# Optimization experiments

Measured on AMD Instinct MI355X. Metric: run time of the kernel, lower is better.

## Reference

```python
import jax, jax.numpy as jnp
import numpy as np

N_HEADS, D_MODEL, DK, DV = 16, 1024, 64, 64
B, S = 4, 2048


def setup_inputs() -> dict:
    key = jax.random.key(0)
    ks = jax.random.split(key, 7)
    scale = 1.0 / np.sqrt(D_MODEL)
    return {
        "Q": jax.random.normal(ks[0], (B, S, D_MODEL), dtype=jnp.float32),
        "K": jax.random.normal(ks[1], (B, S, D_MODEL), dtype=jnp.float32),
        "V": jax.random.normal(ks[2], (B, S, D_MODEL), dtype=jnp.float32),
        # Linear weights stored as [in, out] so y = x @ W (equivalent to torch x @ W.T)
        "w_q": jax.random.normal(ks[3], (D_MODEL, N_HEADS * DK), dtype=jnp.float32) * scale,
        "w_k": jax.random.normal(ks[4], (D_MODEL, N_HEADS * DK), dtype=jnp.float32) * scale,
        "w_v": jax.random.normal(ks[5], (D_MODEL, N_HEADS * DV), dtype=jnp.float32) * scale,
        "w_o": jax.random.normal(ks[6], (N_HEADS * DV, D_MODEL), dtype=jnp.float32) * scale,
    }


def reference(Q, K, V, w_q, w_k, w_v, w_o):
    b, s, _ = Q.shape
    # projections -> [B, H, S, d]
    q = (Q @ w_q).reshape(b, s, N_HEADS, DK).transpose(0, 2, 1, 3)
    k = (K @ w_k).reshape(b, s, N_HEADS, DK).transpose(0, 2, 1, 3)
    v = (V @ w_v).reshape(b, s, N_HEADS, DV).transpose(0, 2, 1, 3)
    # scaled dot-product attention, full [B,H,S,S] scores (matches source)
    scores = jnp.einsum("bhqd,bhkd->bhqk", q, k) / jnp.sqrt(jnp.float32(DK))
    attn = jax.nn.softmax(scores, axis=-1)
    x = jnp.einsum("bhqk,bhkd->bhqd", attn, v)
    x = x.transpose(0, 2, 1, 3).reshape(b, s, N_HEADS * DV)
    return x @ w_o
```

## Files before the change

kernel.cpp:

```cpp
#include <hip/hip_runtime.h>
#include <stdint.h>

#define B_   4
#define S_   2048
#define H_   16
#define D_   64
#define DM_  1024
#define NTOK (B_ * S_)

typedef __attribute__((ext_vector_type(8))) short short8;
typedef __attribute__((ext_vector_type(4))) float floatx4;

__device__ inline unsigned short f2bf(float f) {
  unsigned int u = __float_as_uint(f);
  u += 0x7FFFu + ((u >> 16) & 1u);
  return (unsigned short)(u >> 16);
}

__device__ inline floatx4 mfma_bf16(short8 a, short8 b, floatx4 c) {
  return __builtin_amdgcn_mfma_f32_16x16x32_bf16(a, b, c, 0, 0, 0);
}

__device__ inline unsigned int pack_bf2(float lo, float hi) {
  return __builtin_amdgcn_perm(__float_as_uint(hi), __float_as_uint(lo), 0x07060302u);
}

__device__ inline void gload_lds16(const unsigned short* g, unsigned short* l) {
  __builtin_amdgcn_global_load_lds(
      (const __attribute__((address_space(1))) unsigned int*)g,
      (__attribute__((address_space(3))) unsigned int*)l, 16, 0, 0);
}

__global__ __launch_bounds__(256) void cast3_kernel(const float* __restrict__ Q,
                                                    const float* __restrict__ Kf,
                                                    const float* __restrict__ V,
                                                    unsigned short* __restrict__ qB,
                                                    unsigned short* __restrict__ kB,
                                                    unsigned short* __restrict__ vB) {
  const float* in = blockIdx.z == 0 ? Q : blockIdx.z == 1 ? Kf : V;
  unsigned short* out = blockIdx.z == 0 ? qB : blockIdx.z == 1 ? kB : vB;
  const int n4 = NTOK * DM_ / 4;
  for (int i = blockIdx.x * 256 + threadIdx.x; i < n4; i += gridDim.x * 256) {
    float4 v = ((const float4*)in)[i];
    ushort4 o;
    o.x = f2bf(v.x); o.y = f2bf(v.y); o.z = f2bf(v.z); o.w = f2bf(v.w);
    ((ushort4*)out)[i] = o;
  }
}

__global__ __launch_bounds__(256) void wt_kernel(const float* __restrict__ w0,
                                                 const float* __restrict__ w1,
                                                 const float* __restrict__ w2,
                                                 const float* __restrict__ w3,
                                                 unsigned short* __restrict__ o0,
                                                 unsigned short* __restrict__ o1,
                                                 unsigned short* __restrict__ o2,
                                                 unsigned short* __restrict__ o3) {
  __shared__ unsigned short T[64 * 68];
  const float* w = blockIdx.z == 0 ? w0 : blockIdx.z == 1 ? w1 : blockIdx.z == 2 ? w2 : w3;
  unsigned short* o = blockIdx.z == 0 ? o0 : blockIdx.z == 1 ? o1 : blockIdx.z == 2 ? o2 : o3;
  const int tid = threadIdx.x;
  const int R0 = blockIdx.y * 64;
  const int C0 = blockIdx.x * 64;
  for (int it = 0; it < 16; it++) {
    int lr = it * 4 + (tid >> 6), lc = tid & 63;
    T[lc * 68 + lr] = f2bf(w[(size_t)(R0 + lr) * 1024 + C0 + lc]);
  }
  __syncthreads();
  for (int it = 0; it < 2; it++) {
    int orow = it * 32 + (tid >> 3), oc = (tid & 7) * 8;
    union { ushort4 h[2]; short8 v8; } u;
    u.h[0] = *(const ushort4*)(T + orow * 68 + oc);
    u.h[1] = *(const ushort4*)(T + orow * 68 + oc + 4);
    *(short8*)(o + (size_t)(C0 + orow) * 1024 + R0 + oc) = u.v8;
  }
}

__global__ __launch_bounds__(512) void gemm256_kernel(
    const unsigned short* __restrict__ A0, const unsigned short* __restrict__ A1,
    const unsigned short* __restrict__ A2,
    const unsigned short* __restrict__ Bt0, const unsigned short* __restrict__ Bt1,
    const unsigned short* __restrict__ Bt2,
    void* __restrict__ C0, void* __restrict__ C1, void* __restrict__ C2,
    int mode_z0, float scale_z0) {
  constexpr int K = 1024;
  __shared__ __align__(16) unsigned short As[2][256 * 64];
  __shared__ __align__(16) unsigned short Bs[2][128 * 64];

  const int tid  = threadIdx.x;
  const int wave = tid >> 6, lane = tid & 63;
  const int quad = lane >> 4, l16 = lane & 15;
  const int wm = wave >> 2, wn = wave & 3;

  const int g  = blockIdx.x * gridDim.y + blockIdx.y;
  const int z  = g >> 8;
  const int rz = g & 255;
  const int mb = rz >> 3, nb = rz & 7;
  const int m0 = mb * 256, n0 = nb * 128;

  const unsigned short* A  = z == 0 ? A0  : z == 1 ? A1  : A2;
  const unsigned short* BT = z == 0 ? Bt0 : z == 1 ? Bt1 : Bt2;
  void* Cout               = z == 0 ? C0  : z == 1 ? C1  : C2;
  const int   mode  = z == 0 ? mode_z0 : (z == 2 ? 2 : 0);
  const float scale = z == 0 ? scale_z0 : 1.0f;

  floatx4 acc[8][2] = {};

#define STAGE256(k0, buf)                                              \
  do {                                                                 \
    _Pragma("unroll")                                                  \
    for (int p = 0; p < 4; p++) {                                      \
      int si = p * 512 + tid;                                          \
      int rr = si >> 3;                                                \
      int gc = (si & 7) ^ (rr & 7);                                    \
      gload_lds16(A + (size_t)(m0 + rr) * K + (k0) + gc * 8,           \
                  As[buf] + (size_t)(p * 512 + wave * 64) * 8);        \
    }                                                                  \
    _Pragma("unroll")                                                  \
    for (int p = 0; p < 2; p++) {                                      \
      int si = p * 512 + tid;                                          \
      int rr = si >> 3;                                                \
      int gc = (si & 7) ^ (rr & 7);                                    \
      gload_lds16(BT + (size_t)(n0 + rr) * K + (k0) + gc * 8,          \
                  Bs[buf] + (size_t)(p * 512 + wave * 64) * 8);        \
    }                                                                  \
  } while (0)

  STAGE256(0, 0);

  int cur = 0;
  for (int k0 = 0; k0 < K; k0 += 64) {
    __syncthreads();

    if (k0 + 64 < K) STAGE256(k0 + 64, cur ^ 1);

    short8 bfr[2][2];
#pragma unroll
    for (int n = 0; n < 2; n++)
#pragma unroll
      for (int kk = 0; kk < 2; kk++) {
        int rb = wn * 32 + n * 16 + l16;
        int j = kk * 4 + quad;
        bfr[n][kk] = *(const short8*)(Bs[cur] + rb * 64 + (j ^ (rb & 7)) * 8);
      }
#pragma unroll
    for (int f = 0; f < 8; f++) {
      int ra = wm * 128 + f * 16 + l16;
      short8 a0 = *(const short8*)(As[cur] + ra * 64 + ((quad)     ^ (ra & 7)) * 8);
      short8 a1 = *(const short8*)(As[cur] + ra * 64 + ((4 + quad) ^ (ra & 7)) * 8);
#pragma unroll
      for (int n = 0; n < 2; n++) {
        acc[f][n] = mfma_bf16(a0, bfr[n][0], acc[f][n]);
        acc[f][n] = mfma_bf16(a1, bfr[n][1], acc[f][n]);
      }
    }
    cur ^= 1;
  }
#undef STAGE256

#pragma unroll
  for (int f = 0; f < 8; f++)
#pragma unroll
    for (int n = 0; n < 2; n++)
#pragma unroll
      for (int r = 0; r < 4; r++) {
        int gm = m0 + wm * 128 + f * 16 + quad * 4 + r;
        int gn = n0 + wn * 32 + n * 16 + l16;
        float val = acc[f][n][r] * scale;
        if (mode == 0) {
          int b = gm >> 11, s = gm & 2047;
          int h = gn >> 6,  d = gn & 63;
          ((unsigned short*)Cout)[((size_t)((b * H_ + h) * S_ + s) << 6) + d] = f2bf(val);
        } else if (mode == 1) {
          ((float*)Cout)[((size_t)gm << 10) + gn] = val;
        } else {
          int b = gm >> 11, s = gm & 2047;
          int h = gn >> 6,  d = gn & 63;
          int p = ((s & 63) >> 4) + (s & 15) * 4;
          ((unsigned short*)Cout)[(((size_t)(b * H_ + h) * 64 + d) << 11) + (s & ~63) + p] = f2bf(val);
        }
      }
}

__global__ __launch_bounds__(512, 4) void attn_kernel(const unsigned short* __restrict__ q,
                                                      const unsigned short* __restrict__ k,
                                                      const unsigned short* __restrict__ vT,
                                                      unsigned short* __restrict__ X) {
  __shared__ unsigned short Ks[2][64 * 64];
  __shared__ unsigned short Vt[2][64 * 64];
  __shared__ unsigned short Ps[8][16 * 72];

  const int tid  = threadIdx.x;
  const int wave = tid >> 6, lane = tid & 63;
  const int quad = lane >> 4, l16 = lane & 15;
  const int bh = blockIdx.x * 8 + (blockIdx.y >> 3);
  const int q0 = (blockIdx.y & 7) * 256;

  const unsigned short* qh = q  + (size_t)bh * S_ * 64;
  const unsigned short* kh = k  + (size_t)bh * S_ * 64;
  const unsigned short* vh = vT + (size_t)bh * 64 * S_;

  const int sr  = tid >> 3;
  const int sgc = (tid & 7) ^ (sr & 7);

  short8 qf[2][2];
  for (int qt = 0; qt < 2; qt++) {
    int row = q0 + wave * 32 + qt * 16 + l16;
    for (int kk = 0; kk < 2; kk++)
      qf[qt][kk] = *(const short8*)(qh + (size_t)row * 64 + kk * 32 + quad * 8);
  }

  short8 onesb = {};
  if (l16 == 0)
    for (int e = 0; e < 8; e++) onesb[e] = (short)0x3F80;

  const floatx4 fz = {};
  floatx4 O[2][4] = {};
  floatx4 lacc[2] = {};

  gload_lds16(kh + (size_t)sr * 64 + sgc * 8,       Ks[0] + (size_t)(wave * 64) * 8);
  gload_lds16(vh + (size_t)sr * S_ + 0 + sgc * 8,   Vt[0] + (size_t)(wave * 64) * 8);

  int cur = 0;
  for (int j0 = 0; j0 < S_; j0 += 64) {
    __syncthreads();

    if (j0 + 64 < S_) {
      int nxt = cur ^ 1;
      gload_lds16(kh + (size_t)(j0 + 64 + sr) * 64 + sgc * 8,
                  Ks[nxt] + (size_t)(wave * 64) * 8);
      gload_lds16(vh + (size_t)sr * S_ + (j0 + 64) + sgc * 8,
                  Vt[nxt] + (size_t)(wave * 64) * 8);
    }

    short8 kf[4][2];
    for (int jf = 0; jf < 4; jf++)
      for (int kk = 0; kk < 2; kk++) {
        int sl = (kk * 4 + quad) ^ (l16 & 7);
        kf[jf][kk] = *(const short8*)(Ks[cur] + (jf * 16 + l16) * 64 + sl * 8);
      }

    unsigned short* pw = Ps[wave];
    short8 pa[2][2];
    for (int qt = 0; qt < 2; qt++) {
      floatx4 s[4];
      for (int jf = 0; jf < 4; jf++) {
        s[jf] = mfma_bf16(qf[qt][0], kf[jf][0], fz);
        s[jf] = mfma_bf16(qf[qt][1], kf[jf][1], s[jf]);
      }
      for (int r = 0; r < 4; r++) {
        float e0 = __builtin_amdgcn_exp2f(s[0][r]);
        float e1 = __builtin_amdgcn_exp2f(s[1][r]);
        float e2 = __builtin_amdgcn_exp2f(s[2][r]);
        float e3 = __builtin_amdgcn_exp2f(s[3][r]);
        uint2 pk;
        pk.x = pack_bf2(e0, e1);
        pk.y = pack_bf2(e2, e3);
        *(uint2*)(pw + (quad * 4 + r) * 72 + l16 * 4) = pk;
      }
      pa[qt][0] = *(const short8*)(pw + l16 * 72 + quad * 8);
      pa[qt][1] = *(const short8*)(pw + l16 * 72 + 32 + quad * 8);
      lacc[qt] = mfma_bf16(pa[qt][0], onesb, lacc[qt]);
      lacc[qt] = mfma_bf16(pa[qt][1], onesb, lacc[qt]);
    }

    for (int df = 0; df < 4; df++) {
      int sl0 = quad ^ (l16 & 7);
      int sl1 = (4 + quad) ^ (l16 & 7);
      short8 v0 = *(const short8*)(Vt[cur] + (df * 16 + l16) * 64 + sl0 * 8);
      short8 v1 = *(const short8*)(Vt[cur] + (df * 16 + l16) * 64 + sl1 * 8);
      for (int qt = 0; qt < 2; qt++) {
        O[qt][df] = mfma_bf16(pa[qt][0], v0, O[qt][df]);
        O[qt][df] = mfma_bf16(pa[qt][1], v1, O[qt][df]);
      }
    }
    cur ^= 1;
  }

  const int b = bh >> 4, h = bh & 15;
  for (int qt = 0; qt < 2; qt++)
    for (int r = 0; r < 4; r++) {
      float lsum = __shfl(lacc[qt][r], (lane & 48));
      float inv = 1.0f / lsum;
      int row = q0 + wave * 32 + qt * 16 + quad * 4 + r;
      unsigned short* dst = X + ((size_t)(b * S_ + row) << 10) + h * 64;
      for (int df = 0; df < 4; df++)
        dst[df * 16 + l16] = f2bf(O[qt][df][r] * inv);
    }
}

extern "C" void kernel_launch(void* const* d_in, const int* in_sizes, int n_in,
                              void* d_out, int out_size, void* d_ws, size_t ws_size,
                              hipStream_t stream) {
  const float* Q  = (const float*)d_in[0];
  const float* K  = (const float*)d_in[1];
  const float* V  = (const float*)d_in[2];
  const float* wq = (const float*)d_in[3];
  const float* wk = (const float*)d_in[4];
  const float* wv = (const float*)d_in[5];
  const float* wo = (const float*)d_in[6];

  char* ws = (char*)d_ws;
  unsigned short* buf0 = (unsigned short*)ws;
  unsigned short* wqT  = (unsigned short*)(ws + (size_t)(16 << 20));
  unsigned short* wkT  = (unsigned short*)(ws + (size_t)(18 << 20));
  unsigned short* wvT  = (unsigned short*)(ws + (size_t)(20 << 20));
  unsigned short* woT  = (unsigned short*)(ws + (size_t)(22 << 20));
  unsigned short* qP   = (unsigned short*)(ws + (size_t)(24 << 20));
  unsigned short* kP   = (unsigned short*)(ws + (size_t)(40 << 20));
  unsigned short* vTg  = (unsigned short*)(ws + (size_t)(56 << 20));

  unsigned short* qB = (unsigned short*)d_out;
  unsigned short* kB = qB + (size_t)8 * 1024 * 1024;
  unsigned short* vB = buf0;

  const float SC = 0.18033688011112043f;

  wt_kernel<<<dim3(16, 16, 4), dim3(256), 0, stream>>>(wq, wk, wv, wo, wqT, wkT, wvT, woT);

  cast3_kernel<<<dim3(2048, 1, 3), dim3(256), 0, stream>>>(Q, K, V, qB, kB, vB);

  gemm256_kernel<<<dim3(8, 96), dim3(512), 0, stream>>>(
      qB, kB, vB, wqT, wkT, wvT, qP, kP, vTg, 0, SC);

  attn_kernel<<<dim3(8, 64), dim3(512), 0, stream>>>(qP, kP, vTg, buf0);

  gemm256_kernel<<<dim3(8, 32), dim3(512), 0, stream>>>(
      buf0, buf0, buf0, woT, woT, woT, d_out, d_out, d_out, 1, 1.0f);
}
```

Measured before the change: 357.7 us.

## Triple-buffer GEMM K-loop with explicit vmcnt waits and merge prep kernels

The projection GEMM moves from double to triple buffering in LDS, keeping two K-tiles of global->LDS loads in flight. It replaces __syncthreads with counted s_waitcnt vmcnt plus raw barriers. The weight-transpose and input-cast kernels are fused into one launch to cut launch overhead. LDS use grows to 144KB per block, and the hand-counted waits must match the number of issued loads.

```diff
diff --git a/kernel.cpp b/kernel.cpp
--- a/kernel.cpp
+++ b/kernel.cpp
@@ -31,37 +31,39 @@
       (__attribute__((address_space(3))) unsigned int*)l, 16, 0, 0);
 }
 
-__global__ __launch_bounds__(256) void cast3_kernel(const float* __restrict__ Q,
-                                                    const float* __restrict__ Kf,
-                                                    const float* __restrict__ V,
-                                                    unsigned short* __restrict__ qB,
-                                                    unsigned short* __restrict__ kB,
-                                                    unsigned short* __restrict__ vB) {
-  const float* in = blockIdx.z == 0 ? Q : blockIdx.z == 1 ? Kf : V;
-  unsigned short* out = blockIdx.z == 0 ? qB : blockIdx.z == 1 ? kB : vB;
-  const int n4 = NTOK * DM_ / 4;
-  for (int i = blockIdx.x * 256 + threadIdx.x; i < n4; i += gridDim.x * 256) {
-    float4 v = ((const float4*)in)[i];
-    ushort4 o;
-    o.x = f2bf(v.x); o.y = f2bf(v.y); o.z = f2bf(v.z); o.w = f2bf(v.w);
-    ((ushort4*)out)[i] = o;
-  }
-}
-
-__global__ __launch_bounds__(256) void wt_kernel(const float* __restrict__ w0,
-                                                 const float* __restrict__ w1,
-                                                 const float* __restrict__ w2,
-                                                 const float* __restrict__ w3,
-                                                 unsigned short* __restrict__ o0,
-                                                 unsigned short* __restrict__ o1,
-                                                 unsigned short* __restrict__ o2,
-                                                 unsigned short* __restrict__ o3) {
+__global__ __launch_bounds__(256) void prep_kernel(
+    const float* __restrict__ Q, const float* __restrict__ Kf,
+    const float* __restrict__ V,
+    const float* __restrict__ w0, const float* __restrict__ w1,
+    const float* __restrict__ w2, const float* __restrict__ w3,
+    unsigned short* __restrict__ qB, unsigned short* __restrict__ kB,
+    unsigned short* __restrict__ vB,
+    unsigned short* __restrict__ o0, unsigned short* __restrict__ o1,
+    unsigned short* __restrict__ o2, unsigned short* __restrict__ o3) {
   __shared__ unsigned short T[64 * 68];
-  const float* w = blockIdx.z == 0 ? w0 : blockIdx.z == 1 ? w1 : blockIdx.z == 2 ? w2 : w3;
-  unsigned short* o = blockIdx.z == 0 ? o0 : blockIdx.z == 1 ? o1 : blockIdx.z == 2 ? o2 : o3;
+  const int z = blockIdx.z;
   const int tid = threadIdx.x;
-  const int R0 = blockIdx.y * 64;
-  const int C0 = blockIdx.x * 64;
+
+  if (z < 3) {
+    const float* in = z == 0 ? Q : z == 1 ? Kf : V;
+    unsigned short* out = z == 0 ? qB : z == 1 ? kB : vB;
+    const int n4 = NTOK * DM_ / 4;
+    for (int i = blockIdx.x * 256 + tid; i < n4; i += gridDim.x * 256) {
+      float4 v = ((const float4*)in)[i];
+      ushort4 o;
+      o.x = f2bf(v.x); o.y = f2bf(v.y); o.z = f2bf(v.z); o.w = f2bf(v.w);
+      ((ushort4*)out)[i] = o;
+    }
+    return;
+  }
+
+  const int bx = blockIdx.x;
+  if (bx >= 1024) return;
+  const int wsel = bx >> 8, tile = bx & 255;
+  const float* w = wsel == 0 ? w0 : wsel == 1 ? w1 : wsel == 2 ? w2 : w3;
+  unsigned short* o = wsel == 0 ? o0 : wsel == 1 ? o1 : wsel == 2 ? o2 : o3;
+  const int R0 = (tile >> 4) * 64;
+  const int C0 = (tile & 15) * 64;
   for (int it = 0; it < 16; it++) {
     int lr = it * 4 + (tid >> 6), lc = tid & 63;
     T[lc * 68 + lr] = f2bf(w[(size_t)(R0 + lr) * 1024 + C0 + lc]);
@@ -84,8 +86,9 @@
     void* __restrict__ C0, void* __restrict__ C1, void* __restrict__ C2,
     int mode_z0, float scale_z0) {
   constexpr int K = 1024;
-  __shared__ __align__(16) unsigned short As[2][256 * 64];
-  __shared__ __align__(16) unsigned short Bs[2][128 * 64];
+  constexpr int NKT = K / 64;
+  __shared__ __align__(16) unsigned short As[3][256 * 64];
+  __shared__ __align__(16) unsigned short Bs[3][128 * 64];
 
   const int tid  = threadIdx.x;
   const int wave = tid >> 6, lane = tid & 63;
@@ -106,14 +109,15 @@
 
   floatx4 acc[8][2] = {};
 
-#define STAGE256(k0, buf)                                              \
+#define STAGE256(kt, buf)                                              \
   do {                                                                 \
+    const int k0s = (kt) * 64;                                         \
     _Pragma("unroll")                                                  \
     for (int p = 0; p < 4; p++) {                                      \
       int si = p * 512 + tid;                                          \
       int rr = si >> 3;                                                \
       int gc = (si & 7) ^ (rr & 7);                                    \
-      gload_lds16(A + (size_t)(m0 + rr) * K + (k0) + gc * 8,           \
+      gload_lds16(A + (size_t)(m0 + rr) * K + k0s + gc * 8,            \
                   As[buf] + (size_t)(p * 512 + wave * 64) * 8);        \
     }                                                                  \
     _Pragma("unroll")                                                  \
@@ -121,18 +125,22 @@
       int si = p * 512 + tid;                                          \
       int rr = si >> 3;                                                \
       int gc = (si & 7) ^ (rr & 7);                                    \
-      gload_lds16(BT + (size_t)(n0 + rr) * K + (k0) + gc * 8,          \
+      gload_lds16(BT + (size_t)(n0 + rr) * K + k0s + gc * 8,           \
                   Bs[buf] + (size_t)(p * 512 + wave * 64) * 8);        \
     }                                                                  \
   } while (0)
 
   STAGE256(0, 0);
-
-  int cur = 0;
-  for (int k0 = 0; k0 < K; k0 += 64) {
-    __syncthreads();
-
-    if (k0 + 64 < K) STAGE256(k0 + 64, cur ^ 1);
+  STAGE256(1, 1);
+
+  for (int t = 0; t < NKT; ++t) {
+    const int bi = t % 3;
+    if (t + 2 < NKT) STAGE256(t + 2, (t + 2) % 3);
+
+    if (t < NKT - 2)       asm volatile("s_waitcnt vmcnt(12)" ::: "memory");
+    else if (t == NKT - 2) asm volatile("s_waitcnt vmcnt(6)"  ::: "memory");
+    else                   asm volatile("s_waitcnt vmcnt(0)"  ::: "memory");
+    asm volatile("s_barrier" ::: "memory");
 
     short8 bfr[2][2];
 #pragma unroll
@@ -141,20 +149,21 @@
       for (int kk = 0; kk < 2; kk++) {
         int rb = wn * 32 + n * 16 + l16;
         int j = kk * 4 + quad;
-        bfr[n][kk] = *(const short8*)(Bs[cur] + rb * 64 + (j ^ (rb & 7)) * 8);
+        bfr[n][kk] = *(const short8*)(Bs[bi] + rb * 64 + (j ^ (rb & 7)) * 8);
       }
 #pragma unroll
     for (int f = 0; f < 8; f++) {
       int ra = wm * 128 + f * 16 + l16;
-      short8 a0 = *(const short8*)(As[cur] + ra * 64 + ((quad)     ^ (ra & 7)) * 8);
-      short8 a1 = *(const short8*)(As[cur] + ra * 64 + ((4 + quad) ^ (ra & 7)) * 8);
+      short8 a0 = *(const short8*)(As[bi] + ra * 64 + ((quad)     ^ (ra & 7)) * 8);
+      short8 a1 = *(const short8*)(As[bi] + ra * 64 + ((4 + quad) ^ (ra & 7)) * 8);
 #pragma unroll
       for (int n = 0; n < 2; n++) {
         acc[f][n] = mfma_bf16(a0, bfr[n][0], acc[f][n]);
         acc[f][n] = mfma_bf16(a1, bfr[n][1], acc[f][n]);
       }
     }
-    cur ^= 1;
+
+    asm volatile("s_barrier" ::: "memory");
   }
 #undef STAGE256
 
@@ -316,9 +325,8 @@
 
   const float SC = 0.18033688011112043f;
 
-  wt_kernel<<<dim3(16, 16, 4), dim3(256), 0, stream>>>(wq, wk, wv, wo, wqT, wkT, wvT, woT);
-
-  cast3_kernel<<<dim3(2048, 1, 3), dim3(256), 0, stream>>>(Q, K, V, qB, kB, vB);
+  prep_kernel<<<dim3(2048, 1, 4), dim3(256), 0, stream>>>(
+      Q, K, V, wq, wk, wv, wo, qB, kB, vB, wqT, wkT, wvT, woT);
 
   gemm256_kernel<<<dim3(8, 96), dim3(512), 0, stream>>>(
       qB, kB, vB, wqT, wkT, wvT, qP, kP, vTg, 0, SC);
```

After: 358.3 us. Within noise of the previous version (+0.2%).
